# Optimization experiments

Measured on AMD Instinct MI355X. Metric: run time of the kernel, lower is better.

The kernel has to match this reference:

```python
import jax, jax.numpy as jnp
import numpy as np


def setup_inputs() -> dict:
    key = jax.random.key(0)
    k1, k2 = jax.random.split(key)
    B, N, M = 32, 4096, 4096
    pred = jax.random.normal(k1, (B, N, 3), dtype=jnp.float32)
    target = jax.random.normal(k2, (B, M, 3), dtype=jnp.float32)
    return {"pred": pred, "target": target}


def reference(pred, target):
    # pairwise euclidean distances: [B, N, M]
    # d2 = |p|^2 + |t|^2 - 2 p.t  (matches torch.cdist p=2)
    p2 = jnp.sum(pred * pred, axis=-1)                      # [B, N]
    t2 = jnp.sum(target * target, axis=-1)                  # [B, M]
    pt = jnp.einsum('bnd,bmd->bnm', pred, target)           # [B, N, M]
    d2 = p2[:, :, None] + t2[:, None, :] - 2.0 * pt
    dist = jnp.sqrt(jnp.maximum(d2, 0.0))                   # [B, N, M]
    min_d = jnp.min(dist, axis=2)                           # [B, N]
    return jnp.mean(min_d)
```

## Files before the change

kernel.cpp:

```cpp
#include <hip/hip_runtime.h>


typedef short bf16x8 __attribute__((ext_vector_type(8)));
typedef float f32x16 __attribute__((ext_vector_type(16)));

constexpr int Bc = 32;
constexpr int Nc = 4096;
constexpr int Mc = 4096;
constexpr int BLOCK = 256;
constexpr int PTS = Bc * Nc;

__device__ __forceinline__ unsigned short brne(float x) {
  unsigned u = __float_as_uint(x);
  return (unsigned short)((u + 0x7FFFu + ((u >> 16) & 1u)) >> 16);
}
__device__ __forceinline__ float bf2f(unsigned short h) {
  return __uint_as_float(((unsigned)h) << 16);
}
__device__ __forceinline__ unsigned pack(unsigned short lo, unsigned short hi) {
  return (unsigned)lo | ((unsigned)hi << 16);
}

__global__ __launch_bounds__(BLOCK) void emd_prep_kernel(
    const float* __restrict__ pred, const float* __restrict__ target,
    uint4* __restrict__ A0, uint4* __restrict__ A1,
    uint4* __restrict__ B0, uint4* __restrict__ B1,
    unsigned int* __restrict__ wmin) {
  const int i = blockIdx.x * BLOCK + threadIdx.x;
  const unsigned short ONE = 0x3F80;
  wmin[i] = 0xFFFFFFFFu;
  {
    float x = pred[3 * i], y = pred[3 * i + 1], z = pred[3 * i + 2];
    unsigned short xh = brne(x), xl = brne(x - bf2f(xh));
    unsigned short yh = brne(y), yl = brne(y - bf2f(yh));
    unsigned short zh = brne(z), zl = brne(z - bf2f(zh));
    float p2 = fmaf(x, x, fmaf(y, y, z * z));
    unsigned short ph = brne(p2), pl = brne(p2 - bf2f(ph));
    A0[i] = make_uint4(pack(xh, xh), pack(xl, yh), pack(yh, yl), pack(zh, zh));
    A1[i] = make_uint4(pack(zl, ph), pack(pl, ONE), pack(ONE, 0), 0);
  }
  {
    float x = -2.0f * target[3 * i], y = -2.0f * target[3 * i + 1],
          z = -2.0f * target[3 * i + 2];
    unsigned short xh = brne(x), xl = brne(x - bf2f(xh));
    unsigned short yh = brne(y), yl = brne(y - bf2f(yh));
    unsigned short zh = brne(z), zl = brne(z - bf2f(zh));
    float t2 = 0.25f * fmaf(x, x, fmaf(y, y, z * z));
    unsigned short th = brne(t2), tl = brne(t2 - bf2f(th));
    B0[i] = make_uint4(pack(xh, xl), pack(xh, yh), pack(yl, yh), pack(zh, zl));
    B1[i] = make_uint4(pack(zh, ONE), pack(ONE, th), pack(tl, 0), 0);
  }
}

__global__ __launch_bounds__(BLOCK)
__attribute__((amdgpu_waves_per_eu(4, 4)))
void emd_main_kernel(
    const uint4* __restrict__ A0, const uint4* __restrict__ A1,
    const uint4* __restrict__ B0, const uint4* __restrict__ B1,
    unsigned int* __restrict__ wmin) {
  __shared__ uint4 ldsb[2048];

  const int b = blockIdx.x >> 5;
  const int pg = (blockIdx.x >> 1) & 15;
  const int th = blockIdx.x & 1;
  const int lane = threadIdx.x & 63;
  const int half = lane >> 5;
  const int l31 = lane & 31;
  const int wave = threadIdx.x >> 6;

  const uint4* Ap = half ? A1 : A0;
  const size_t abase = (size_t)b * Nc + pg * 256 + wave * 64 + l31;
  uint4 a0u = Ap[abase];
  uint4 a1u = Ap[abase + 32];
  bf16x8 a0 = *(const bf16x8*)&a0u;
  bf16x8 a1 = *(const bf16x8*)&a1u;

  f32x16 r0, r1;
#pragma unroll
  for (int i = 0; i < 16; ++i) { r0[i] = 3.4e38f; r1[i] = 3.4e38f; }

  for (int c = 0; c < 2; ++c) {
    __syncthreads();
    const size_t tb = (size_t)b * Mc + th * 2048 + c * 1024;
    const uint4* s0 = B0 + tb;
    const uint4* s1 = B1 + tb;
#pragma unroll
    for (int i = 0; i < 4; ++i)
      ldsb[threadIdx.x + i * BLOCK] = s0[threadIdx.x + i * BLOCK];
#pragma unroll
    for (int i = 0; i < 4; ++i)
      ldsb[1024 + threadIdx.x + i * BLOCK] = s1[threadIdx.x + i * BLOCK];
    __syncthreads();

    const int base = half * 1024 + l31;
#pragma unroll 2
    for (int t = 0; t < 32; t += 2) {
      uint4 bu0 = ldsb[base + t * 32];
      uint4 bu1 = ldsb[base + (t + 1) * 32];
      bf16x8 bf0 = *(const bf16x8*)&bu0;
      bf16x8 bf1 = *(const bf16x8*)&bu1;
      f32x16 z{};
      f32x16 d00 = __builtin_amdgcn_mfma_f32_32x32x16_bf16(a0, bf0, z, 0, 0, 0);
      f32x16 d01 = __builtin_amdgcn_mfma_f32_32x32x16_bf16(a0, bf1, z, 0, 0, 0);
      f32x16 d10 = __builtin_amdgcn_mfma_f32_32x32x16_bf16(a1, bf0, z, 0, 0, 0);
      f32x16 d11 = __builtin_amdgcn_mfma_f32_32x32x16_bf16(a1, bf1, z, 0, 0, 0);
#pragma unroll
      for (int i = 0; i < 16; ++i) {
        r0[i] = fminf(fminf(d00[i], d01[i]), r0[i]);
        r1[i] = fminf(fminf(d10[i], d11[i]), r1[i]);
      }
    }
  }

#pragma unroll
  for (int off = 1; off < 32; off <<= 1) {
#pragma unroll
    for (int i = 0; i < 16; ++i) {
      r0[i] = fminf(r0[i], __shfl_xor(r0[i], off, 64));
      r1[i] = fminf(r1[i], __shfl_xor(r1[i], off, 64));
    }
  }
  if (l31 == 0) {
    const int pbase = b * Nc + pg * 256 + wave * 64;
#pragma unroll
    for (int i = 0; i < 16; ++i) {
      const int row = (i & 3) + 8 * (i >> 2) + 4 * half;
      atomicMin(&wmin[pbase + row], __float_as_uint(fmaxf(r0[i], 0.0f)));
      atomicMin(&wmin[pbase + 32 + row], __float_as_uint(fmaxf(r1[i], 0.0f)));
    }
  }
}

__global__ __launch_bounds__(BLOCK) void emd_finish_kernel(
    const uint4* __restrict__ wmin, float* __restrict__ out) {
  __shared__ float wsum[4];
  const int i = blockIdx.x * BLOCK + threadIdx.x;
  uint4 v = wmin[i];
  float s = sqrtf(__uint_as_float(v.x)) + sqrtf(__uint_as_float(v.y)) +
            sqrtf(__uint_as_float(v.z)) + sqrtf(__uint_as_float(v.w));
#pragma unroll
  for (int off = 32; off > 0; off >>= 1) s += __shfl_down(s, off, 64);
  if ((threadIdx.x & 63) == 0) wsum[threadIdx.x >> 6] = s;
  __syncthreads();
  if (threadIdx.x == 0) {
    float tot = (wsum[0] + wsum[1]) + (wsum[2] + wsum[3]);
    atomicAdd(out, tot * (1.0f / (float)PTS));
  }
}

extern "C" void kernel_launch(void* const* d_in, const int* in_sizes, int n_in,
                              void* d_out, int out_size, void* d_ws, size_t ws_size,
                              hipStream_t stream) {
  const float* pred = (const float*)d_in[0];
  const float* target = (const float*)d_in[1];
  float* out = (float*)d_out;

  char* w = (char*)d_ws;
  uint4* A0 = (uint4*)(w + 0 * (size_t)PTS * 16);
  uint4* A1 = (uint4*)(w + 1 * (size_t)PTS * 16);
  uint4* B0 = (uint4*)(w + 2 * (size_t)PTS * 16);
  uint4* B1 = (uint4*)(w + 3 * (size_t)PTS * 16);
  unsigned int* wmin = (unsigned int*)(w + 4 * (size_t)PTS * 16);

  emd_prep_kernel<<<dim3(PTS / BLOCK), dim3(BLOCK), 0, stream>>>(
      pred, target, A0, A1, B0, B1, wmin);
  emd_main_kernel<<<dim3(Bc * 16 * 2), dim3(BLOCK), 0, stream>>>(
      A0, A1, B0, B1, wmin);
  emd_finish_kernel<<<dim3(PTS / 4 / BLOCK), dim3(BLOCK), 0, stream>>>(
      (const uint4*)wmin, out);
}
```

Before: 87.60 us.

## Fuse bf16 split-precision prep into main kernel and replace atomics with slices

Removes the separate prep kernel. Pred and target points are now converted to hi/lo bf16 operands directly in the main kernel: pred goes through LDS, and target is converted while staging into LDS. Each of the two M-halves writes its per-row minima to its own slice instead of using atomicMin on a pre-initialized buffer. The finish kernel then takes the min of the two slices before the sqrt. This drops one launch, the 8 MB workspace round-trip and the atomics. In exchange, the conversion arithmetic is repeated across the 16 point-group blocks that read each target tile, and the global target loads are strided 12-byte reads.

```diff
diff --git a/kernel.cpp b/kernel.cpp
--- a/kernel.cpp
+++ b/kernel.cpp
@@ -21,44 +21,13 @@
   return (unsigned)lo | ((unsigned)hi << 16);
 }
 
-__global__ __launch_bounds__(BLOCK) void emd_prep_kernel(
-    const float* __restrict__ pred, const float* __restrict__ target,
-    uint4* __restrict__ A0, uint4* __restrict__ A1,
-    uint4* __restrict__ B0, uint4* __restrict__ B1,
-    unsigned int* __restrict__ wmin) {
-  const int i = blockIdx.x * BLOCK + threadIdx.x;
-  const unsigned short ONE = 0x3F80;
-  wmin[i] = 0xFFFFFFFFu;
-  {
-    float x = pred[3 * i], y = pred[3 * i + 1], z = pred[3 * i + 2];
-    unsigned short xh = brne(x), xl = brne(x - bf2f(xh));
-    unsigned short yh = brne(y), yl = brne(y - bf2f(yh));
-    unsigned short zh = brne(z), zl = brne(z - bf2f(zh));
-    float p2 = fmaf(x, x, fmaf(y, y, z * z));
-    unsigned short ph = brne(p2), pl = brne(p2 - bf2f(ph));
-    A0[i] = make_uint4(pack(xh, xh), pack(xl, yh), pack(yh, yl), pack(zh, zh));
-    A1[i] = make_uint4(pack(zl, ph), pack(pl, ONE), pack(ONE, 0), 0);
-  }
-  {
-    float x = -2.0f * target[3 * i], y = -2.0f * target[3 * i + 1],
-          z = -2.0f * target[3 * i + 2];
-    unsigned short xh = brne(x), xl = brne(x - bf2f(xh));
-    unsigned short yh = brne(y), yl = brne(y - bf2f(yh));
-    unsigned short zh = brne(z), zl = brne(z - bf2f(zh));
-    float t2 = 0.25f * fmaf(x, x, fmaf(y, y, z * z));
-    unsigned short th = brne(t2), tl = brne(t2 - bf2f(th));
-    B0[i] = make_uint4(pack(xh, xl), pack(xh, yh), pack(yl, yh), pack(zh, zl));
-    B1[i] = make_uint4(pack(zh, ONE), pack(ONE, th), pack(tl, 0), 0);
-  }
-}
-
 __global__ __launch_bounds__(BLOCK)
 __attribute__((amdgpu_waves_per_eu(4, 4)))
-void emd_main_kernel(
-    const uint4* __restrict__ A0, const uint4* __restrict__ A1,
-    const uint4* __restrict__ B0, const uint4* __restrict__ B1,
-    unsigned int* __restrict__ wmin) {
+void emd_main_kernel(const float* __restrict__ pred,
+                     const float* __restrict__ target,
+                     float* __restrict__ slices) {
   __shared__ uint4 ldsb[2048];
+  __shared__ uint4 ldsa[512];
 
   const int b = blockIdx.x >> 5;
   const int pg = (blockIdx.x >> 1) & 15;
@@ -67,11 +36,25 @@
   const int half = lane >> 5;
   const int l31 = lane & 31;
   const int wave = threadIdx.x >> 6;
+  const unsigned short ONE = 0x3F80;
 
-  const uint4* Ap = half ? A1 : A0;
-  const size_t abase = (size_t)b * Nc + pg * 256 + wave * 64 + l31;
-  uint4 a0u = Ap[abase];
-  uint4 a1u = Ap[abase + 32];
+  {
+    const size_t i = (size_t)b * Nc + pg * 256 + threadIdx.x;
+    float x = pred[3 * i], y = pred[3 * i + 1], z = pred[3 * i + 2];
+    unsigned short xh = brne(x), xl = brne(x - bf2f(xh));
+    unsigned short yh = brne(y), yl = brne(y - bf2f(yh));
+    unsigned short zh = brne(z), zl = brne(z - bf2f(zh));
+    float p2 = fmaf(x, x, fmaf(y, y, z * z));
+    unsigned short ph = brne(p2), pl = brne(p2 - bf2f(ph));
+    ldsa[threadIdx.x] =
+        make_uint4(pack(xh, xh), pack(xl, yh), pack(yh, yl), pack(zh, zh));
+    ldsa[256 + threadIdx.x] =
+        make_uint4(pack(zl, ph), pack(pl, ONE), pack(ONE, 0), 0);
+  }
+  __syncthreads();
+
+  uint4 a0u = ldsa[half * 256 + wave * 64 + l31];
+  uint4 a1u = ldsa[half * 256 + wave * 64 + 32 + l31];
   bf16x8 a0 = *(const bf16x8*)&a0u;
   bf16x8 a1 = *(const bf16x8*)&a1u;
 
@@ -81,15 +64,22 @@
 
   for (int c = 0; c < 2; ++c) {
     __syncthreads();
-    const size_t tb = (size_t)b * Mc + th * 2048 + c * 1024;
-    const uint4* s0 = B0 + tb;
-    const uint4* s1 = B1 + tb;
+    const size_t tbase = (size_t)b * Mc + th * 2048 + c * 1024;
 #pragma unroll
-    for (int i = 0; i < 4; ++i)
-      ldsb[threadIdx.x + i * BLOCK] = s0[threadIdx.x + i * BLOCK];
-#pragma unroll
-    for (int i = 0; i < 4; ++i)
-      ldsb[1024 + threadIdx.x + i * BLOCK] = s1[threadIdx.x + i * BLOCK];
+    for (int j = 0; j < 4; ++j) {
+      const int pt = threadIdx.x + j * BLOCK;
+      const float* tp = target + (tbase + pt) * 3;
+      float x = -2.0f * tp[0], y = -2.0f * tp[1], z = -2.0f * tp[2];
+      unsigned short xh = brne(x), xl = brne(x - bf2f(xh));
+      unsigned short yh = brne(y), yl = brne(y - bf2f(yh));
+      unsigned short zh = brne(z), zl = brne(z - bf2f(zh));
+      float t2 = 0.25f * fmaf(x, x, fmaf(y, y, z * z));
+      unsigned short t2h = brne(t2), t2l = brne(t2 - bf2f(t2h));
+      ldsb[pt] =
+          make_uint4(pack(xh, xl), pack(xh, yh), pack(yl, yh), pack(zh, zl));
+      ldsb[1024 + pt] =
+          make_uint4(pack(zh, ONE), pack(ONE, t2h), pack(t2l, 0), 0);
+    }
     __syncthreads();
 
     const int base = half * 1024 + l31;
@@ -121,23 +111,24 @@
     }
   }
   if (l31 == 0) {
-    const int pbase = b * Nc + pg * 256 + wave * 64;
+    float* sl = slices + (size_t)th * PTS + b * Nc + pg * 256 + wave * 64;
 #pragma unroll
     for (int i = 0; i < 16; ++i) {
       const int row = (i & 3) + 8 * (i >> 2) + 4 * half;
-      atomicMin(&wmin[pbase + row], __float_as_uint(fmaxf(r0[i], 0.0f)));
-      atomicMin(&wmin[pbase + 32 + row], __float_as_uint(fmaxf(r1[i], 0.0f)));
+      sl[row] = fmaxf(r0[i], 0.0f);
+      sl[32 + row] = fmaxf(r1[i], 0.0f);
     }
   }
 }
 
 __global__ __launch_bounds__(BLOCK) void emd_finish_kernel(
-    const uint4* __restrict__ wmin, float* __restrict__ out) {
+    const float4* __restrict__ slices, float* __restrict__ out) {
   __shared__ float wsum[4];
   const int i = blockIdx.x * BLOCK + threadIdx.x;
-  uint4 v = wmin[i];
-  float s = sqrtf(__uint_as_float(v.x)) + sqrtf(__uint_as_float(v.y)) +
-            sqrtf(__uint_as_float(v.z)) + sqrtf(__uint_as_float(v.w));
+  float4 v0 = slices[i];
+  float4 v1 = slices[PTS / 4 + i];
+  float s = sqrtf(fminf(v0.x, v1.x)) + sqrtf(fminf(v0.y, v1.y)) +
+            sqrtf(fminf(v0.z, v1.z)) + sqrtf(fminf(v0.w, v1.w));
 #pragma unroll
   for (int off = 32; off > 0; off >>= 1) s += __shfl_down(s, off, 64);
   if ((threadIdx.x & 63) == 0) wsum[threadIdx.x >> 6] = s;
@@ -154,18 +145,10 @@
   const float* pred = (const float*)d_in[0];
   const float* target = (const float*)d_in[1];
   float* out = (float*)d_out;
+  float* slices = (float*)d_ws;
 
-  char* w = (char*)d_ws;
-  uint4* A0 = (uint4*)(w + 0 * (size_t)PTS * 16);
-  uint4* A1 = (uint4*)(w + 1 * (size_t)PTS * 16);
-  uint4* B0 = (uint4*)(w + 2 * (size_t)PTS * 16);
-  uint4* B1 = (uint4*)(w + 3 * (size_t)PTS * 16);
-  unsigned int* wmin = (unsigned int*)(w + 4 * (size_t)PTS * 16);
-
-  emd_prep_kernel<<<dim3(PTS / BLOCK), dim3(BLOCK), 0, stream>>>(
-      pred, target, A0, A1, B0, B1, wmin);
   emd_main_kernel<<<dim3(Bc * 16 * 2), dim3(BLOCK), 0, stream>>>(
-      A0, A1, B0, B1, wmin);
+      pred, target, slices);
   emd_finish_kernel<<<dim3(PTS / 4 / BLOCK), dim3(BLOCK), 0, stream>>>(
-      (const uint4*)wmin, out);
+      (const float4*)slices, out);
 }
```

Measured after the change: 80.57 us. 1.09x faster.
